# Optimization experiments

Measured on AMD Instinct MI355X. Metric: run time of the kernel, lower is better.

Reference implementation:

```python
import jax, jax.numpy as jnp
import numpy as np

H, DM, DX = 4, 64, 64  # num_heads, out_m_dim, out_x_dim
IN_L, IN_M, IN_X = 128, 128, 128
N, E, E2 = 10000, 160000, 320000


def _edge_softmax(scores, dst, num_nodes):
    # scores: [n_edges, H, 1]; softmax over edges sharing the same dst node
    mx = jax.ops.segment_max(scores, dst, num_segments=num_nodes)
    ex = jnp.exp(scores - mx[dst])
    denom = jax.ops.segment_sum(ex, dst, num_segments=num_nodes)
    return ex / denom[dst]


def setup_inputs() -> dict:
    key = jax.random.key(0)
    ks = jax.random.split(key, 24)

    def xn(k, shape):
        fan = sum(shape)
        return jax.random.normal(k, shape, dtype=jnp.float32) * np.sqrt(2.0 / fan)

    inp = {
        'l_feats': jax.random.normal(ks[0], (N, IN_L), dtype=jnp.float32),
        'm_feats': jax.random.normal(ks[1], (E, IN_M), dtype=jnp.float32),
        'x_feats': jax.random.normal(ks[2], (E2, IN_X), dtype=jnp.float32),
        'g_src': jax.random.randint(ks[3], (E,), 0, N, dtype=jnp.int32),
        'g_dst': jax.random.randint(ks[4], (E,), 0, N, dtype=jnp.int32),
        'lg_src': jax.random.randint(ks[5], (E2,), 0, E, dtype=jnp.int32),
        'lg_dst': jax.random.randint(ks[6], (E2,), 0, E, dtype=jnp.int32),
        # line-graph branch params (torch Linear convention: W [out, in])
        'W_lg_node': xn(ks[7], (DM * H, IN_M + IN_X)),
        'b_lg_node': jnp.zeros((DM * H,), dtype=jnp.float32),
        'W_lg_ni': xn(ks[8], (DX * H, IN_M)),
        'W_lg_fij': xn(ks[9], (DX * H, IN_X)),
        'W_lg_nj': xn(ks[10], (DX * H, IN_M)),
        'lg_attn': xn(ks[11], (1, H, DX)),
        'bias_lg': jnp.zeros((H * DX,), dtype=jnp.float32),
        # base-graph branch params
        'W_g_node': xn(ks[12], (DM * H, IN_M + IN_L)),
        'b_g_node': jnp.zeros((DM * H,), dtype=jnp.float32),
        'W_g_ni': xn(ks[13], (DM * H, IN_L)),
        'W_g_fij': xn(ks[14], (DM * H, IN_M)),
        'W_g_nj': xn(ks[15], (DM * H, IN_L)),
        'g_attn': xn(ks[16], (1, H, DM)),
        'bias_g': jnp.zeros((H * DM,), dtype=jnp.float32),
    }
    return inp


def reference(l_feats, m_feats, x_feats,
              W_lg_node, b_lg_node, W_lg_ni, W_lg_fij, W_lg_nj, lg_attn, bias_lg,
              W_g_node, b_g_node, W_g_ni, W_g_fij, W_g_nj, g_attn, bias_g,
              g_src, g_dst, lg_src, lg_dst):
    n_nodes = l_feats.shape[0]      # graph nodes
    n_lnodes = m_feats.shape[0]     # l_graph nodes == graph edges
    lrelu = jax.nn.leaky_relu       # slope 0.01 (torch default)

    # ---- line-graph attention branch ----
    lg_f_ni = m_feats @ W_lg_ni.T                      # [E, H*DX]
    lg_f_nj = m_feats @ W_lg_nj.T
    lg_f_fij = x_feats @ W_lg_fij.T                    # [E2, H*DX]
    lg_f_out = lrelu(lg_f_ni[lg_src] + lg_f_nj[lg_dst] + lg_f_fij + bias_lg)
    xr = lg_f_out.reshape(-1, H, DX)                   # [E2, H, DX]
    lg_e = jnp.sum(xr * lg_attn, axis=-1, keepdims=True)  # [E2, H, 1]
    a_lg = _edge_softmax(lg_e, lg_dst, n_lnodes)       # [E2, H, 1]

    # mean-aggregate l_graph edge feats onto dst nodes (DGL send_and_recv mean)
    cnt = jax.ops.segment_sum(jnp.ones((lg_dst.shape[0],), dtype=x_feats.dtype),
                              lg_dst, num_segments=n_lnodes)
    agg = jax.ops.segment_sum(x_feats, lg_dst, num_segments=n_lnodes)
    agg = agg / jnp.maximum(cnt, 1.0)[:, None]         # [E, IN_X]

    m1 = jnp.concatenate([m_feats, agg], axis=1)       # [E, IN_M+IN_X]
    h1 = (m1 @ W_lg_node.T + b_lg_node).reshape(-1, H, DM)
    msg1 = h1[lg_src] * a_lg                           # u_mul_e
    h1_dst = jax.ops.segment_sum(msg1, lg_dst, num_segments=n_lnodes)
    lg_h_out = jnp.sum(lrelu(h1_dst), axis=1)          # [E, DM]

    # ---- base-graph attention branch ----
    g_f_ni = l_feats @ W_g_ni.T                        # [N, H*DM]
    g_f_nj = l_feats @ W_g_nj.T
    g_f_fij = m_feats @ W_g_fij.T                      # [E, H*DM]
    g_f_out = lrelu(g_f_ni[g_src] + g_f_nj[g_dst] + g_f_fij + bias_g)
    g_f_out = g_f_out.reshape(-1, H, DM)               # [E, H, DM]
    g_e = jnp.sum(g_f_out * g_attn, axis=-1, keepdims=True)  # [E, H, 1]

    node_edge = l_feats[g_src] + l_feats[g_dst]        # [E, IN_L]
    m2 = jnp.concatenate([node_edge, m_feats], axis=1)  # [E, IN_L+IN_M]
    h2 = (m2 @ W_g_node.T + b_g_node).reshape(-1, H, DM)
    a_g = _edge_softmax(g_e, g_dst, n_nodes)           # [E, H, 1] (per graph edge)
    # l_graph.update_all(u_mul_v): msg[e2] = h2[src(e2)] * a_g[dst(e2)]
    msg2 = h2[lg_src] * a_g[lg_dst]
    h2_dst = jax.ops.segment_sum(msg2, lg_dst, num_segments=n_lnodes)
    g_h_out = jnp.sum(lrelu(h2_dst), axis=1)           # [E, DM]

    return g_h_out + lg_h_out                          # [E, DM]
```

## Files before the change

kernel.cpp:

```cpp
#include <hip/hip_runtime.h>
#include <math.h>

#define LRELU(x) ((x) > 0.0f ? (x) : 0.01f * (x))

typedef __attribute__((ext_vector_type(8))) short short8;
typedef __attribute__((ext_vector_type(4))) float f32x4;

__device__ __forceinline__ unsigned fenc(float f) {
    unsigned u = __float_as_uint(f);
    return (u & 0x80000000u) ? ~u : (u | 0x80000000u);
}
__device__ __forceinline__ float fdec(unsigned u) {
    return __uint_as_float((u & 0x80000000u) ? (u & 0x7FFFFFFFu) : ~u);
}
__device__ __forceinline__ unsigned short f2bf(float f) {
    unsigned u = __float_as_uint(f);
    u += 0x7FFFu + ((u >> 16) & 1u);
    return (unsigned short)(u >> 16);
}
__device__ __forceinline__ float bf2f(unsigned short b) {
    return __uint_as_float(((unsigned)b) << 16);
}
__device__ __forceinline__ ushort4 cvt4(float4 v) {
    ushort4 p;
    p.x = f2bf(v.x); p.y = f2bf(v.y); p.z = f2bf(v.z); p.w = f2bf(v.w);
    return p;
}

__global__ __launch_bounds__(256) void f2bf_k(
    const float* __restrict__ in, unsigned short* __restrict__ out, int n)
{
    for (int i = blockIdx.x * 256 + threadIdx.x; i < n; i += gridDim.x * 256)
        out[i] = f2bf(in[i]);
}

__global__ __launch_bounds__(256) void gemm128_mfma(
    const float* __restrict__ A, const unsigned short* __restrict__ Wbf,
    const float* __restrict__ biasf, unsigned short* __restrict__ Cout, int M)
{
    __shared__ __align__(16) unsigned short smem[64 * 264];
    const int row0 = blockIdx.x * 64;
    const int tid = threadIdx.x;
    const int wv = tid >> 6, lane = tid & 63;
    const int ln = lane & 15, quad = lane >> 4;

#pragma unroll 1
    for (int i = tid; i < 2048; i += 256) {
        int row = i >> 5, c4 = (i & 31) * 4;
        int r = row0 + row;
        float4 v = make_float4(0.f, 0.f, 0.f, 0.f);
        if (r < M) v = *(const float4*)&A[(size_t)r * 128 + c4];
        *(ushort4*)&smem[row * 136 + c4] = cvt4(v);
    }
    __syncthreads();

    f32x4 acc[16];
#pragma unroll
    for (int t = 0; t < 16; ++t) acc[t] = (f32x4){0.f, 0.f, 0.f, 0.f};

#pragma unroll 1
    for (int ks = 0; ks < 4; ++ks) {
        short8 a = *(const short8*)&smem[(wv * 16 + ln) * 136 + ks * 32 + quad * 8];
#pragma unroll
        for (int t = 0; t < 16; ++t) {
            short8 b = *(const short8*)&Wbf[(size_t)(t * 16 + ln) * 128 + ks * 32 + quad * 8];
            acc[t] = __builtin_amdgcn_mfma_f32_16x16x32_bf16(a, b, acc[t], 0, 0, 0);
        }
    }
    __syncthreads();

#pragma unroll
    for (int t = 0; t < 16; ++t) {
        int col = t * 16 + ln;
        float bb = biasf ? biasf[col] : 0.0f;
#pragma unroll
        for (int rg = 0; rg < 4; ++rg)
            smem[(wv * 16 + quad * 4 + rg) * 264 + col] = f2bf(acc[t][rg] + bb);
    }
    __syncthreads();
#pragma unroll 1
    for (int i = tid; i < 2048; i += 256) {
        int row = i >> 5, c8 = (i & 31) * 8;
        int r = row0 + row;
        if (r < M) *(short8*)&Cout[(size_t)r * 256 + c8] = *(const short8*)&smem[row * 264 + c8];
    }
}

__global__ __launch_bounds__(256) void gemm_score_mfma(
    const float* __restrict__ A, const unsigned short* __restrict__ Wbf,
    const unsigned short* __restrict__ fni, const unsigned short* __restrict__ fnj,
    const float* __restrict__ bias, const float* __restrict__ attn,
    const int* __restrict__ src, const int* __restrict__ dst,
    float* __restrict__ ebuf, unsigned* __restrict__ smax, int M, int domax)
{
    __shared__ __align__(16) unsigned short smem[64 * 264];
    const int row0 = blockIdx.x * 64;
    const int tid = threadIdx.x;
    const int wv = tid >> 6, lane = tid & 63;
    const int ln = lane & 15, quad = lane >> 4;

#pragma unroll 1
    for (int i = tid; i < 2048; i += 256) {
        int row = i >> 5, c4 = (i & 31) * 4;
        int r = row0 + row;
        float4 v = make_float4(0.f, 0.f, 0.f, 0.f);
        if (r < M) v = *(const float4*)&A[(size_t)r * 128 + c4];
        *(ushort4*)&smem[row * 136 + c4] = cvt4(v);
    }
    __syncthreads();

    f32x4 acc[16];
#pragma unroll
    for (int t = 0; t < 16; ++t) acc[t] = (f32x4){0.f, 0.f, 0.f, 0.f};

#pragma unroll 1
    for (int ks = 0; ks < 4; ++ks) {
        short8 a = *(const short8*)&smem[(wv * 16 + ln) * 136 + ks * 32 + quad * 8];
#pragma unroll
        for (int t = 0; t < 16; ++t) {
            short8 b = *(const short8*)&Wbf[(size_t)(t * 16 + ln) * 128 + ks * 32 + quad * 8];
            acc[t] = __builtin_amdgcn_mfma_f32_16x16x32_bf16(a, b, acc[t], 0, 0, 0);
        }
    }
    __syncthreads();

#pragma unroll
    for (int t = 0; t < 16; ++t) {
        int col = t * 16 + ln;
#pragma unroll
        for (int rg = 0; rg < 4; ++rg)
            smem[(wv * 16 + quad * 4 + rg) * 264 + col] = f2bf(acc[t][rg]);
    }

    const int c4 = lane * 4;
    const float4 bias4 = *(const float4*)&bias[c4];
    const float4 attn4 = *(const float4*)&attn[c4];

#pragma unroll 4
    for (int i = 0; i < 16; ++i) {
        int rr = wv * 16 + i;
        int r = row0 + rr;
        if (r >= M) continue;
        int s = src[r], d = dst[r];
        ushort4 f4 = *(const ushort4*)&smem[rr * 264 + c4];
        ushort4 u4 = *(const ushort4*)&fni[(size_t)s * 256 + c4];
        ushort4 v4 = *(const ushort4*)&fnj[(size_t)d * 256 + c4];
        float p = 0.f;
        {
            float v0 = bf2f(f4.x) + bf2f(u4.x) + bf2f(v4.x) + bias4.x;
            float v1 = bf2f(f4.y) + bf2f(u4.y) + bf2f(v4.y) + bias4.y;
            float v2 = bf2f(f4.z) + bf2f(u4.z) + bf2f(v4.z) + bias4.z;
            float v3 = bf2f(f4.w) + bf2f(u4.w) + bf2f(v4.w) + bias4.w;
            p = LRELU(v0) * attn4.x + LRELU(v1) * attn4.y
              + LRELU(v2) * attn4.z + LRELU(v3) * attn4.w;
        }
        p += __shfl_xor(p, 1, 64);
        p += __shfl_xor(p, 2, 64);
        p += __shfl_xor(p, 4, 64);
        p += __shfl_xor(p, 8, 64);
        if (ln == 0) {
            ebuf[(size_t)r * 4 + quad] = p;
            if (domax) atomicMax(&smax[(size_t)d * 4 + quad], fenc(p));
        }
    }
}

__global__ __launch_bounds__(256) void gemm256_mfma(
    const float* __restrict__ A0, const void* __restrict__ A1v,
    const int* __restrict__ gsrc, const int* __restrict__ gdst,
    const unsigned short* __restrict__ Wbf, const float* __restrict__ biasf,
    unsigned short* __restrict__ Cout, int M, int mode)
{
    __shared__ __align__(16) unsigned short smem[64 * 264];
    const int row0 = blockIdx.x * 64;
    const int tid = threadIdx.x;
    const int wv = tid >> 6, lane = tid & 63;
    const int ln = lane & 15, quad = lane >> 4;

    if (mode == 0) {
        const unsigned short* A1 = (const unsigned short*)A1v;
#pragma unroll 1
        for (int i = tid; i < 2048; i += 256) {
            int row = i >> 5, c4 = (i & 31) * 4;
            int r = row0 + row;
            float4 v = make_float4(0.f, 0.f, 0.f, 0.f);
            if (r < M) v = *(const float4*)&A0[(size_t)r * 128 + c4];
            *(ushort4*)&smem[row * 264 + c4] = cvt4(v);
        }
#pragma unroll 1
        for (int i = tid; i < 1024; i += 256) {
            int row = i >> 4, c8 = (i & 15) * 8;
            int r = row0 + row;
            short8 v;
#pragma unroll
            for (int q = 0; q < 8; ++q) v[q] = 0;
            if (r < M) v = *(const short8*)&A1[(size_t)r * 128 + c8];
            *(short8*)&smem[row * 264 + 128 + c8] = v;
        }
    } else {
        const float* A1 = (const float*)A1v;
#pragma unroll 1
        for (int i = tid; i < 2048; i += 256) {
            int row = i >> 5, c4 = (i & 31) * 4;
            int r = row0 + row;
            float4 v = make_float4(0.f, 0.f, 0.f, 0.f);
            if (r < M) {
                float4 a = *(const float4*)&A0[(size_t)gsrc[r] * 128 + c4];
                float4 b = *(const float4*)&A0[(size_t)gdst[r] * 128 + c4];
                v = make_float4(a.x + b.x, a.y + b.y, a.z + b.z, a.w + b.w);
            }
            *(ushort4*)&smem[row * 264 + c4] = cvt4(v);
        }
#pragma unroll 1
        for (int i = tid; i < 2048; i += 256) {
            int row = i >> 5, c4 = (i & 31) * 4;
            int r = row0 + row;
            float4 v = make_float4(0.f, 0.f, 0.f, 0.f);
            if (r < M) v = *(const float4*)&A1[(size_t)r * 128 + c4];
            *(ushort4*)&smem[row * 264 + 128 + c4] = cvt4(v);
        }
    }
    __syncthreads();

    f32x4 acc[16];
#pragma unroll
    for (int t = 0; t < 16; ++t) acc[t] = (f32x4){0.f, 0.f, 0.f, 0.f};

#pragma unroll 1
    for (int ks = 0; ks < 8; ++ks) {
        short8 a = *(const short8*)&smem[(wv * 16 + ln) * 264 + ks * 32 + quad * 8];
#pragma unroll
        for (int t = 0; t < 16; ++t) {
            short8 b = *(const short8*)&Wbf[(size_t)(t * 16 + ln) * 256 + ks * 32 + quad * 8];
            acc[t] = __builtin_amdgcn_mfma_f32_16x16x32_bf16(a, b, acc[t], 0, 0, 0);
        }
    }
    __syncthreads();

#pragma unroll
    for (int t = 0; t < 16; ++t) {
        int col = t * 16 + ln;
        float bb = biasf[col];
#pragma unroll
        for (int rg = 0; rg < 4; ++rg)
            smem[(wv * 16 + quad * 4 + rg) * 264 + col] = f2bf(acc[t][rg] + bb);
    }
    __syncthreads();
#pragma unroll 1
    for (int i = tid; i < 2048; i += 256) {
        int row = i >> 5, c8 = (i & 31) * 8;
        int r = row0 + row;
        if (r < M) *(short8*)&Cout[(size_t)r * 256 + c8] = *(const short8*)&smem[row * 264 + c8];
    }
}

__global__ __launch_bounds__(256) void edge_exp(
    float* __restrict__ ebuf, const unsigned* __restrict__ smax,
    float* __restrict__ sden, const int* __restrict__ dst, int nE)
{
    int i = blockIdx.x * 256 + threadIdx.x;
    if (i >= nE * 4) return;
    int e = i >> 2, h = i & 3;
    int d = dst[e];
    float m = fdec(smax[(size_t)d * 4 + h]);
    float ex = expf(ebuf[i] - m);
    ebuf[i] = ex;
    atomicAdd(&sden[(size_t)d * 4 + h], ex);
}

__global__ __launch_bounds__(256) void count_k(
    const int* __restrict__ dst, int* __restrict__ cnt, int n)
{
    int i = blockIdx.x * 256 + threadIdx.x;
    if (i < n) atomicAdd(&cnt[dst[i]], 1);
}

__global__ __launch_bounds__(256) void scan1(
    const int* __restrict__ cnt, int* __restrict__ excl, int* __restrict__ bsum, int n)
{
    __shared__ int sd[256];
    int tid = threadIdx.x;
    int i = blockIdx.x * 256 + tid;
    int v = (i < n) ? cnt[i] : 0;
    sd[tid] = v;
    __syncthreads();
    for (int off2 = 1; off2 < 256; off2 <<= 1) {
        int t = (tid >= off2) ? sd[tid - off2] : 0;
        __syncthreads();
        sd[tid] += t;
        __syncthreads();
    }
    if (i < n) excl[i] = sd[tid] - v;
    if (tid == 255) bsum[blockIdx.x] = sd[255];
}

__global__ __launch_bounds__(1024) void scan2(int* __restrict__ bsum, int nb)
{
    __shared__ int sd[1024];
    int tid = threadIdx.x;
    int v = (tid < nb) ? bsum[tid] : 0;
    sd[tid] = v;
    __syncthreads();
    for (int off2 = 1; off2 < 1024; off2 <<= 1) {
        int t = (tid >= off2) ? sd[tid - off2] : 0;
        __syncthreads();
        sd[tid] += t;
        __syncthreads();
    }
    if (tid < nb) bsum[tid] = sd[tid] - v;
}

__global__ __launch_bounds__(256) void scan3(
    int* __restrict__ excl, const int* __restrict__ bsum, int n, int total)
{
    int i = blockIdx.x * 256 + threadIdx.x;
    if (i < n) excl[i] += bsum[i >> 8];
    if (i == 0) excl[n] = total;
}

__global__ __launch_bounds__(256) void fill_k(
    const int* __restrict__ dst, const int* __restrict__ row_ptr,
    int* __restrict__ cursor, int* __restrict__ colidx, int n)
{
    int i = blockIdx.x * 256 + threadIdx.x;
    if (i >= n) return;
    int d = dst[i];
    int p = atomicAdd(&cursor[d], 1);
    colidx[row_ptr[d] + p] = i;
}

__global__ __launch_bounds__(256) void agg_gather(
    const int* __restrict__ row_ptr, const int* __restrict__ colidx,
    const float* __restrict__ x, unsigned short* __restrict__ aggbf, int nE)
{
    const int lane = threadIdx.x & 63;
    const int d = blockIdx.x * 4 + (threadIdx.x >> 6);
    if (d >= nE) return;
    int b = row_ptr[d], en = row_ptr[d + 1];
    float s0 = 0.f, s1 = 0.f;
    for (int k = b; k < en; ++k) {
        int e = colidx[k];
        float2 v = *(const float2*)&x[(size_t)e * 128 + lane * 2];
        s0 += v.x; s1 += v.y;
    }
    float c = fmaxf((float)(en - b), 1.0f);
    ushort2 o;
    o.x = f2bf(s0 / c); o.y = f2bf(s1 / c);
    *(ushort2*)&aggbf[(size_t)d * 128 + lane * 2] = o;
}

__global__ __launch_bounds__(256) void final_agg(
    const int* __restrict__ row_ptr, const int* __restrict__ colidx,
    const int* __restrict__ lg_src, const float* __restrict__ e_lg,
    const unsigned short* __restrict__ h1, const unsigned short* __restrict__ h2,
    const float* __restrict__ e_g, const float* __restrict__ gden,
    const int* __restrict__ g_dst, float* __restrict__ out, int nE)
{
    const int lane = threadIdx.x & 63;
    const int d = blockIdx.x * 4 + (threadIdx.x >> 6);
    if (d >= nE) return;
    int b = row_ptr[d], en = row_ptr[d + 1];

    float mx0 = -1e30f, mx1 = -1e30f, mx2 = -1e30f, mx3 = -1e30f;
    for (int k = b; k < en; ++k) {
        float4 sc = *(const float4*)&e_lg[(size_t)colidx[k] * 4];
        mx0 = fmaxf(mx0, sc.x); mx1 = fmaxf(mx1, sc.y);
        mx2 = fmaxf(mx2, sc.z); mx3 = fmaxf(mx3, sc.w);
    }
    float den0 = 0.f, den1 = 0.f, den2 = 0.f, den3 = 0.f;
    float a10 = 0.f, a11 = 0.f, a12 = 0.f, a13 = 0.f;
    float a20 = 0.f, a21 = 0.f, a22 = 0.f, a23 = 0.f;
    for (int k = b; k < en; ++k) {
        int e = colidx[k];
        float4 sc = *(const float4*)&e_lg[(size_t)e * 4];
        float w0 = expf(sc.x - mx0), w1 = expf(sc.y - mx1);
        float w2 = expf(sc.z - mx2), w3 = expf(sc.w - mx3);
        den0 += w0; den1 += w1; den2 += w2; den3 += w3;
        int s = lg_src[e];
        const unsigned short* p1 = &h1[(size_t)s * 256 + lane];
        const unsigned short* p2 = &h2[(size_t)s * 256 + lane];
        a10 += bf2f(p1[0])   * w0;
        a11 += bf2f(p1[64])  * w1;
        a12 += bf2f(p1[128]) * w2;
        a13 += bf2f(p1[192]) * w3;
        a20 += bf2f(p2[0]);
        a21 += bf2f(p2[64]);
        a22 += bf2f(p2[128]);
        a23 += bf2f(p2[192]);
    }
    float o = 0.f;
    if (en > b) {
        float v0 = a10 / den0, v1 = a11 / den1, v2 = a12 / den2, v3 = a13 / den3;
        o += LRELU(v0) + LRELU(v1) + LRELU(v2) + LRELU(v3);
    }
    int gd = g_dst[d];
    float g0 = e_g[(size_t)d * 4 + 0] / gden[(size_t)gd * 4 + 0] * a20;
    float g1 = e_g[(size_t)d * 4 + 1] / gden[(size_t)gd * 4 + 1] * a21;
    float g2 = e_g[(size_t)d * 4 + 2] / gden[(size_t)gd * 4 + 2] * a22;
    float g3 = e_g[(size_t)d * 4 + 3] / gden[(size_t)gd * 4 + 3] * a23;
    o += LRELU(g0) + LRELU(g1) + LRELU(g2) + LRELU(g3);
    out[(size_t)d * 64 + lane] = o;
}

extern "C" void kernel_launch(void* const* d_in, const int* in_sizes, int n_in,
                              void* d_out, int out_size, void* d_ws, size_t ws_size,
                              hipStream_t stream)
{
    const float* l_feats   = (const float*)d_in[0];
    const float* m_feats   = (const float*)d_in[1];
    const float* x_feats   = (const float*)d_in[2];
    const int*   g_src     = (const int*)d_in[3];
    const int*   g_dst     = (const int*)d_in[4];
    const int*   lg_src    = (const int*)d_in[5];
    const int*   lg_dst    = (const int*)d_in[6];
    const float* W_lg_node = (const float*)d_in[7];
    const float* b_lg_node = (const float*)d_in[8];
    const float* W_lg_ni   = (const float*)d_in[9];
    const float* W_lg_fij  = (const float*)d_in[10];
    const float* W_lg_nj   = (const float*)d_in[11];
    const float* lg_attn   = (const float*)d_in[12];
    const float* bias_lg   = (const float*)d_in[13];
    const float* W_g_node  = (const float*)d_in[14];
    const float* b_g_node  = (const float*)d_in[15];
    const float* W_g_ni    = (const float*)d_in[16];
    const float* W_g_fij   = (const float*)d_in[17];
    const float* W_g_nj    = (const float*)d_in[18];
    const float* g_attn    = (const float*)d_in[19];
    const float* bias_g    = (const float*)d_in[20];

    const int N  = in_sizes[0] / 128;
    const int E  = in_sizes[3];
    const int E2 = in_sizes[5];

    float* ws = (float*)d_ws;
    size_t off = 0;
    auto alloc = [&](size_t n) { float* p = ws + off; off += n; return p; };

    unsigned short* wbuf = (unsigned short*)alloc(163840);
    unsigned short* wgni_bf    = wbuf;
    unsigned short* wgnj_bf    = wbuf + 32768;
    unsigned short* wlgni_bf   = wbuf + 65536;
    unsigned short* wlgnj_bf   = wbuf + 98304;
    unsigned short* wlgfij_bf  = wbuf + 131072;
    unsigned short* wgfij_bf   = wbuf + 163840;
    unsigned short* wlgnode_bf = wbuf + 196608;
    unsigned short* wgnode_bf  = wbuf + 262144;

    unsigned short* ni_lg = (unsigned short*)alloc((size_t)E * 128);
    unsigned short* nj_lg = (unsigned short*)alloc((size_t)E * 128);
    unsigned short* gni   = (unsigned short*)alloc((size_t)N * 128);
    unsigned short* gnj   = (unsigned short*)alloc((size_t)N * 128);
    unsigned short* aggbf = (unsigned short*)alloc((size_t)E * 64);
    float* e_lg  = alloc((size_t)E2 * 4);
    float* e_g   = alloc((size_t)E * 4);
    unsigned* gmax = (unsigned*)alloc((size_t)N * 4);
    float* gden  = alloc((size_t)N * 4);
    int* row_ptr = (int*)alloc((size_t)E + 4);
    int* colidx  = (int*)alloc((size_t)E2);
    int* cnt     = (int*)alloc((size_t)E);
    int* cursor  = (int*)alloc((size_t)E);
    int* bsum    = (int*)alloc(1024);

    unsigned short* h1 = ni_lg;
    unsigned short* h2 = nj_lg;

    (void)n_in; (void)out_size; (void)ws_size;
    float* outp = (float*)d_out;
    dim3 blk(256);

    hipMemsetAsync(cnt,    0, (size_t)E * 4, stream);
    hipMemsetAsync(cursor, 0, (size_t)E * 4, stream);
    hipMemsetAsync(gmax,   0, (size_t)N * 4 * 4, stream);
    hipMemsetAsync(gden,   0, (size_t)N * 4 * 4, stream);

    f2bf_k<<<128, blk, 0, stream>>>(W_g_ni,    wgni_bf,    32768);
    f2bf_k<<<128, blk, 0, stream>>>(W_g_nj,    wgnj_bf,    32768);
    f2bf_k<<<128, blk, 0, stream>>>(W_lg_ni,   wlgni_bf,   32768);
    f2bf_k<<<128, blk, 0, stream>>>(W_lg_nj,   wlgnj_bf,   32768);
    f2bf_k<<<128, blk, 0, stream>>>(W_lg_fij,  wlgfij_bf,  32768);
    f2bf_k<<<128, blk, 0, stream>>>(W_g_fij,   wgfij_bf,   32768);
    f2bf_k<<<256, blk, 0, stream>>>(W_lg_node, wlgnode_bf, 65536);
    f2bf_k<<<256, blk, 0, stream>>>(W_g_node,  wgnode_bf,  65536);

    const int nb = (E + 255) / 256;
    count_k<<<(E2 + 255) / 256, blk, 0, stream>>>(lg_dst, cnt, E2);
    scan1<<<nb, blk, 0, stream>>>(cnt, row_ptr, bsum, E);
    scan2<<<1, 1024, 0, stream>>>(bsum, nb);
    scan3<<<nb, blk, 0, stream>>>(row_ptr, bsum, E, E2);
    fill_k<<<(E2 + 255) / 256, blk, 0, stream>>>(lg_dst, row_ptr, cursor, colidx, E2);

    gemm128_mfma<<<(N + 63) / 64, blk, 0, stream>>>(l_feats, wgni_bf, nullptr, gni, N);
    gemm128_mfma<<<(N + 63) / 64, blk, 0, stream>>>(l_feats, wgnj_bf, nullptr, gnj, N);
    gemm128_mfma<<<(E + 63) / 64, blk, 0, stream>>>(m_feats, wlgni_bf, nullptr, ni_lg, E);
    gemm128_mfma<<<(E + 63) / 64, blk, 0, stream>>>(m_feats, wlgnj_bf, nullptr, nj_lg, E);

    gemm_score_mfma<<<(E2 + 63) / 64, blk, 0, stream>>>(
        x_feats, wlgfij_bf, ni_lg, nj_lg, bias_lg, lg_attn, lg_src, lg_dst,
        e_lg, nullptr, E2, 0);
    gemm_score_mfma<<<(E + 63) / 64, blk, 0, stream>>>(
        m_feats, wgfij_bf, gni, gnj, bias_g, g_attn, g_src, g_dst,
        e_g, gmax, E, 1);

    edge_exp<<<(unsigned)(((long long)E * 4 + 255) / 256), blk, 0, stream>>>(e_g, gmax, gden, g_dst, E);

    agg_gather<<<(E + 3) / 4, blk, 0, stream>>>(row_ptr, colidx, x_feats, aggbf, E);

    gemm256_mfma<<<(E + 63) / 64, blk, 0, stream>>>(
        m_feats, (const void*)aggbf, nullptr, nullptr, wlgnode_bf, b_lg_node, h1, E, 0);
    gemm256_mfma<<<(E + 63) / 64, blk, 0, stream>>>(
        l_feats, (const void*)m_feats, g_src, g_dst, wgnode_bf, b_g_node, h2, E, 1);

    final_agg<<<(E + 3) / 4, blk, 0, stream>>>(
        row_ptr, colidx, lg_src, e_lg, h1, h2, e_g, gden, g_dst, outp, E);
}
```

Baseline: 1.642 ms.

## Batch global loads in GEMM staging, prefetch gathers, compute line-graph max atomically

The GEMM kernels' A-tile staging loops are unrolled so every global load is issued before any conversion and shared-memory store, which raises memory-level parallelism. In the score kernel, src/dst indices are loaded once per lane and broadcast with shuffles, and the fni/fnj gathers for all 16 rows are issued before the MFMA result is written to shared memory. The line-graph score kernel now also records a per-destination max with atomicMax, so final_agg no longer needs its separate max pass over the edge scores. In exchange this uses more registers, which may cut occupancy, and adds 320k atomics plus a memset.

```diff
diff --git a/kernel.cpp b/kernel.cpp
--- a/kernel.cpp
+++ b/kernel.cpp
@@ -44,13 +44,18 @@
     const int wv = tid >> 6, lane = tid & 63;
     const int ln = lane & 15, quad = lane >> 4;
 
-#pragma unroll 1
-    for (int i = tid; i < 2048; i += 256) {
-        int row = i >> 5, c4 = (i & 31) * 4;
-        int r = row0 + row;
-        float4 v = make_float4(0.f, 0.f, 0.f, 0.f);
-        if (r < M) v = *(const float4*)&A[(size_t)r * 128 + c4];
-        *(ushort4*)&smem[row * 136 + c4] = cvt4(v);
+    float4 va[8];
+#pragma unroll
+    for (int k = 0; k < 8; ++k) {
+        int i = tid + k * 256;
+        int r = row0 + (i >> 5);
+        va[k] = make_float4(0.f, 0.f, 0.f, 0.f);
+        if (r < M) va[k] = *(const float4*)&A[(size_t)r * 128 + (i & 31) * 4];
+    }
+#pragma unroll
+    for (int k = 0; k < 8; ++k) {
+        int i = tid + k * 256;
+        *(ushort4*)&smem[(i >> 5) * 136 + (i & 31) * 4] = cvt4(va[k]);
     }
     __syncthreads();
 
@@ -99,13 +104,23 @@
     const int wv = tid >> 6, lane = tid & 63;
     const int ln = lane & 15, quad = lane >> 4;
 
-#pragma unroll 1
-    for (int i = tid; i < 2048; i += 256) {
-        int row = i >> 5, c4 = (i & 31) * 4;
-        int r = row0 + row;
-        float4 v = make_float4(0.f, 0.f, 0.f, 0.f);
-        if (r < M) v = *(const float4*)&A[(size_t)r * 128 + c4];
-        *(ushort4*)&smem[row * 136 + c4] = cvt4(v);
+    const int rbase = row0 + wv * 16;
+    int myr = rbase + ln;
+    int msrc = 0, mdst = 0;
+    if (myr < M) { msrc = src[myr]; mdst = dst[myr]; }
+
+    float4 va[8];
+#pragma unroll
+    for (int k = 0; k < 8; ++k) {
+        int i = tid + k * 256;
+        int r = row0 + (i >> 5);
+        va[k] = make_float4(0.f, 0.f, 0.f, 0.f);
+        if (r < M) va[k] = *(const float4*)&A[(size_t)r * 128 + (i & 31) * 4];
+    }
+#pragma unroll
+    for (int k = 0; k < 8; ++k) {
+        int i = tid + k * 256;
+        *(ushort4*)&smem[(i >> 5) * 136 + (i & 31) * 4] = cvt4(va[k]);
     }
     __syncthreads();
 
@@ -124,43 +139,47 @@
     }
     __syncthreads();
 
-#pragma unroll
-    for (int t = 0; t < 16; ++t) {
-        int col = t * 16 + ln;
-#pragma unroll
-        for (int rg = 0; rg < 4; ++rg)
-            smem[(wv * 16 + quad * 4 + rg) * 264 + col] = f2bf(acc[t][rg]);
-    }
-
     const int c4 = lane * 4;
     const float4 bias4 = *(const float4*)&bias[c4];
     const float4 attn4 = *(const float4*)&attn[c4];
 
-#pragma unroll 4
+    ushort4 pu[16], pv[16];
+#pragma unroll
+    for (int j = 0; j < 16; ++j) {
+        int s_ = __shfl(msrc, j, 16);
+        int d_ = __shfl(mdst, j, 16);
+        pu[j] = *(const ushort4*)&fni[(size_t)s_ * 256 + c4];
+        pv[j] = *(const ushort4*)&fnj[(size_t)d_ * 256 + c4];
+    }
+
+#pragma unroll
+    for (int t = 0; t < 16; ++t) {
+        int col = t * 16 + ln;
+#pragma unroll
+        for (int rg = 0; rg < 4; ++rg)
+            smem[(wv * 16 + quad * 4 + rg) * 264 + col] = f2bf(acc[t][rg]);
+    }
+
+#pragma unroll
     for (int i = 0; i < 16; ++i) {
         int rr = wv * 16 + i;
         int r = row0 + rr;
         if (r >= M) continue;
-        int s = src[r], d = dst[r];
+        int dIdx = __shfl(mdst, i, 16);
         ushort4 f4 = *(const ushort4*)&smem[rr * 264 + c4];
-        ushort4 u4 = *(const ushort4*)&fni[(size_t)s * 256 + c4];
-        ushort4 v4 = *(const ushort4*)&fnj[(size_t)d * 256 + c4];
-        float p = 0.f;
-        {
-            float v0 = bf2f(f4.x) + bf2f(u4.x) + bf2f(v4.x) + bias4.x;
-            float v1 = bf2f(f4.y) + bf2f(u4.y) + bf2f(v4.y) + bias4.y;
-            float v2 = bf2f(f4.z) + bf2f(u4.z) + bf2f(v4.z) + bias4.z;
-            float v3 = bf2f(f4.w) + bf2f(u4.w) + bf2f(v4.w) + bias4.w;
-            p = LRELU(v0) * attn4.x + LRELU(v1) * attn4.y
-              + LRELU(v2) * attn4.z + LRELU(v3) * attn4.w;
-        }
+        float v0 = bf2f(f4.x) + bf2f(pu[i].x) + bf2f(pv[i].x) + bias4.x;
+        float v1 = bf2f(f4.y) + bf2f(pu[i].y) + bf2f(pv[i].y) + bias4.y;
+        float v2 = bf2f(f4.z) + bf2f(pu[i].z) + bf2f(pv[i].z) + bias4.z;
+        float v3 = bf2f(f4.w) + bf2f(pu[i].w) + bf2f(pv[i].w) + bias4.w;
+        float p = LRELU(v0) * attn4.x + LRELU(v1) * attn4.y
+                + LRELU(v2) * attn4.z + LRELU(v3) * attn4.w;
         p += __shfl_xor(p, 1, 64);
         p += __shfl_xor(p, 2, 64);
         p += __shfl_xor(p, 4, 64);
         p += __shfl_xor(p, 8, 64);
         if (ln == 0) {
             ebuf[(size_t)r * 4 + quad] = p;
-            if (domax) atomicMax(&smax[(size_t)d * 4 + quad], fenc(p));
+            if (domax) atomicMax(&smax[(size_t)dIdx * 4 + quad], fenc(p));
         }
     }
 }
@@ -179,45 +198,64 @@
 
     if (mode == 0) {
         const unsigned short* A1 = (const unsigned short*)A1v;
-#pragma unroll 1
-        for (int i = tid; i < 2048; i += 256) {
-            int row = i >> 5, c4 = (i & 31) * 4;
-            int r = row0 + row;
-            float4 v = make_float4(0.f, 0.f, 0.f, 0.f);
-            if (r < M) v = *(const float4*)&A0[(size_t)r * 128 + c4];
-            *(ushort4*)&smem[row * 264 + c4] = cvt4(v);
-        }
-#pragma unroll 1
-        for (int i = tid; i < 1024; i += 256) {
-            int row = i >> 4, c8 = (i & 15) * 8;
-            int r = row0 + row;
-            short8 v;
-#pragma unroll
-            for (int q = 0; q < 8; ++q) v[q] = 0;
-            if (r < M) v = *(const short8*)&A1[(size_t)r * 128 + c8];
-            *(short8*)&smem[row * 264 + 128 + c8] = v;
+        float4 va[8];
+#pragma unroll
+        for (int k = 0; k < 8; ++k) {
+            int i = tid + k * 256;
+            int r = row0 + (i >> 5);
+            va[k] = make_float4(0.f, 0.f, 0.f, 0.f);
+            if (r < M) va[k] = *(const float4*)&A0[(size_t)r * 128 + (i & 31) * 4];
+        }
+        short8 vb[4];
+#pragma unroll
+        for (int k = 0; k < 4; ++k) {
+            int i = tid + k * 256;
+            int r = row0 + (i >> 4);
+#pragma unroll
+            for (int q = 0; q < 8; ++q) vb[k][q] = 0;
+            if (r < M) vb[k] = *(const short8*)&A1[(size_t)r * 128 + (i & 15) * 8];
+        }
+#pragma unroll
+        for (int k = 0; k < 8; ++k) {
+            int i = tid + k * 256;
+            *(ushort4*)&smem[(i >> 5) * 264 + (i & 31) * 4] = cvt4(va[k]);
+        }
+#pragma unroll
+        for (int k = 0; k < 4; ++k) {
+            int i = tid + k * 256;
+            *(short8*)&smem[(i >> 4) * 264 + 128 + (i & 15) * 8] = vb[k];
         }
     } else {
         const float* A1 = (const float*)A1v;
-#pragma unroll 1
-        for (int i = tid; i < 2048; i += 256) {
-            int row = i >> 5, c4 = (i & 31) * 4;
-            int r = row0 + row;
-            float4 v = make_float4(0.f, 0.f, 0.f, 0.f);
-            if (r < M) {
-                float4 a = *(const float4*)&A0[(size_t)gsrc[r] * 128 + c4];
-                float4 b = *(const float4*)&A0[(size_t)gdst[r] * 128 + c4];
-                v = make_float4(a.x + b.x, a.y + b.y, a.z + b.z, a.w + b.w);
-            }
-            *(ushort4*)&smem[row * 264 + c4] = cvt4(v);
-        }
-#pragma unroll 1
-        for (int i = tid; i < 2048; i += 256) {
-            int row = i >> 5, c4 = (i & 31) * 4;
-            int r = row0 + row;
-            float4 v = make_float4(0.f, 0.f, 0.f, 0.f);
-            if (r < M) v = *(const float4*)&A1[(size_t)r * 128 + c4];
-            *(ushort4*)&smem[row * 264 + 128 + c4] = cvt4(v);
+        int is[8], id[8];
+#pragma unroll
+        for (int k = 0; k < 8; ++k) {
+            int i = tid + k * 256;
+            int r = row0 + (i >> 5);
+            is[k] = (r < M) ? gsrc[r] : 0;
+            id[k] = (r < M) ? gdst[r] : 0;
+        }
+        float4 va[8], vb2[8], vc[8];
+#pragma unroll
+        for (int k = 0; k < 8; ++k) {
+            int i = tid + k * 256;
+            int r = row0 + (i >> 5);
+            int c4i = (i & 31) * 4;
+            va[k]  = *(const float4*)&A0[(size_t)is[k] * 128 + c4i];
+            vb2[k] = *(const float4*)&A0[(size_t)id[k] * 128 + c4i];
+            vc[k] = make_float4(0.f, 0.f, 0.f, 0.f);
+            if (r < M) vc[k] = *(const float4*)&A1[(size_t)r * 128 + c4i];
+        }
+#pragma unroll
+        for (int k = 0; k < 8; ++k) {
+            int i = tid + k * 256;
+            int r = row0 + (i >> 5);
+            int c4i = (i & 31) * 4;
+            float4 v = make_float4(va[k].x + vb2[k].x, va[k].y + vb2[k].y,
+                                   va[k].z + vb2[k].z, va[k].w + vb2[k].w);
+            if (r >= M) v = make_float4(0.f, 0.f, 0.f, 0.f);
+            *(ushort4*)&smem[(i >> 5) * 264 + c4i] = cvt4(v);
+            *(ushort4*)&smem[(i >> 5) * 264 + 128 + c4i] = cvt4(vc[k]);
         }
     }
     __syncthreads();
@@ -352,6 +390,7 @@
 __global__ __launch_bounds__(256) void final_agg(
     const int* __restrict__ row_ptr, const int* __restrict__ colidx,
     const int* __restrict__ lg_src, const float* __restrict__ e_lg,
+    const unsigned* __restrict__ lgmax,
     const unsigned short* __restrict__ h1, const unsigned short* __restrict__ h2,
     const float* __restrict__ e_g, const float* __restrict__ gden,
     const int* __restrict__ g_dst, float* __restrict__ out, int nE)
@@ -361,12 +400,9 @@
     if (d >= nE) return;
     int b = row_ptr[d], en = row_ptr[d + 1];
 
-    float mx0 = -1e30f, mx1 = -1e30f, mx2 = -1e30f, mx3 = -1e30f;
-    for (int k = b; k < en; ++k) {
-        float4 sc = *(const float4*)&e_lg[(size_t)colidx[k] * 4];
-        mx0 = fmaxf(mx0, sc.x); mx1 = fmaxf(mx1, sc.y);
-        mx2 = fmaxf(mx2, sc.z); mx3 = fmaxf(mx3, sc.w);
-    }
+    uint4 mu = *(const uint4*)&lgmax[(size_t)d * 4];
+    float mx0 = fdec(mu.x), mx1 = fdec(mu.y), mx2 = fdec(mu.z), mx3 = fdec(mu.w);
+
     float den0 = 0.f, den1 = 0.f, den2 = 0.f, den3 = 0.f;
     float a10 = 0.f, a11 = 0.f, a12 = 0.f, a13 = 0.f;
     float a20 = 0.f, a21 = 0.f, a22 = 0.f, a23 = 0.f;
@@ -455,6 +491,7 @@
     float* e_g   = alloc((size_t)E * 4);
     unsigned* gmax = (unsigned*)alloc((size_t)N * 4);
     float* gden  = alloc((size_t)N * 4);
+    unsigned* lgmax = (unsigned*)alloc((size_t)E * 4);
     int* row_ptr = (int*)alloc((size_t)E + 4);
     int* colidx  = (int*)alloc((size_t)E2);
     int* cnt     = (int*)alloc((size_t)E);
@@ -472,6 +509,7 @@
     hipMemsetAsync(cursor, 0, (size_t)E * 4, stream);
     hipMemsetAsync(gmax,   0, (size_t)N * 4 * 4, stream);
     hipMemsetAsync(gden,   0, (size_t)N * 4 * 4, stream);
+    hipMemsetAsync(lgmax,  0, (size_t)E * 4 * 4, stream);
 
     f2bf_k<<<128, blk, 0, stream>>>(W_g_ni,    wgni_bf,    32768);
     f2bf_k<<<128, blk, 0, stream>>>(W_g_nj,    wgnj_bf,    32768);
@@ -496,7 +534,7 @@
 
     gemm_score_mfma<<<(E2 + 63) / 64, blk, 0, stream>>>(
         x_feats, wlgfij_bf, ni_lg, nj_lg, bias_lg, lg_attn, lg_src, lg_dst,
-        e_lg, nullptr, E2, 0);
+        e_lg, lgmax, E2, 1);
     gemm_score_mfma<<<(E + 63) / 64, blk, 0, stream>>>(
         m_feats, wgfij_bf, gni, gnj, bias_g, g_attn, g_src, g_dst,
         e_g, gmax, E, 1);
@@ -511,5 +549,5 @@
         l_feats, (const void*)m_feats, g_src, g_dst, wgnode_bf, b_g_node, h2, E, 1);
 
     final_agg<<<(E + 3) / 4, blk, 0, stream>>>(
-        row_ptr, colidx, lg_src, e_lg, h1, h2, e_g, gden, g_dst, outp, E);
-}
+        row_ptr, colidx, lg_src, e_lg, lgmax, h1, h2, e_g, gden, g_dst, outp, E);
+}
```

Result: faster. 1.446 ms (-11.9%).
